# Performance work log

Measured on AMD Instinct MI355X. Metric: run time of the kernel, lower is better.

The kernel has to match this reference:

```python
import jax, jax.numpy as jnp
import numpy as np

B, D, H = 16384, 64, 128
L = D - 1  # number of per-dimension sub-networks (layers 1..dim-1)
W_SCALE = 0.05  # keep alpha outputs small so exp(alpha) stays well-conditioned


def setup_inputs() -> dict:
    key = jax.random.key(0)
    ks = jax.random.split(key, 8)
    return {
        "x": jax.random.normal(ks[0], (B, D), dtype=jnp.float32),
        "W1": jax.random.normal(ks[1], (L, D - 1, H), dtype=jnp.float32) * W_SCALE,
        "b1": jax.random.normal(ks[2], (L, H), dtype=jnp.float32) * W_SCALE,
        "W2": jax.random.normal(ks[3], (L, H, H), dtype=jnp.float32) * W_SCALE,
        "b2": jax.random.normal(ks[4], (L, H), dtype=jnp.float32) * W_SCALE,
        "W3": jax.random.normal(ks[5], (L, H, 2), dtype=jnp.float32) * W_SCALE,
        "b3": jax.random.normal(ks[6], (L, 2), dtype=jnp.float32) * W_SCALE,
        "initial_param": jax.random.uniform(
            ks[7], (2,), dtype=jnp.float32,
            minval=-np.sqrt(0.5), maxval=np.sqrt(0.5)),
    }


def reference(x, W1, b1, W2, b2, W3, b3, initial_param):
    # x: [B, D]. Layer l (l=0..L-1) corresponds to dim i=l+1 and consumes
    # x[:, :l+1]; we realize the ragged inputs via a triangular mask on W1.
    b, d = x.shape
    # mask[l, j] = 1 if input feature j is visible to layer l (j <= l)
    mask = (jnp.arange(d - 1)[None, :] <= jnp.arange(L)[:, None]).astype(x.dtype)
    W1m = W1 * mask[:, :, None]                       # [L, D-1, H]
    h = jnp.tanh(jnp.einsum('bd,ldh->blh', x[:, :d - 1], W1m) + b1)  # [B, L, H]
    h = jnp.tanh(jnp.einsum('blh,lhk->blk', h, W2) + b2)             # [B, L, H]
    out = jnp.einsum('blh,lho->blo', h, W3) + b3                     # [B, L, 2]
    mu0 = jnp.broadcast_to(initial_param[0], (b, 1))
    a0 = jnp.broadcast_to(initial_param[1], (b, 1))
    mu = jnp.concatenate([mu0, out[..., 0]], axis=1)   # [B, D]
    alpha = jnp.concatenate([a0, out[..., 1]], axis=1)  # [B, D]
    z = (x - mu) * jnp.exp(-alpha)
    log_det = -jnp.sum(alpha, axis=1)                  # [B]
    return z[:, ::-1], log_det
```

## Files before the change

### kernel.cpp

```cpp
#include <hip/hip_runtime.h>
#include <hip/hip_bf16.h>
#include <stdint.h>

#define B_N   16384
#define D_N   64
#define L_N   63
#define H_N   128
#define K2LOG2E 2.8853900817779268f

typedef unsigned int   u32;
typedef unsigned short u16;
typedef __attribute__((ext_vector_type(8))) __bf16 bf16x8;
typedef __attribute__((ext_vector_type(4))) float  f32x4;

__device__ __forceinline__ u16 f2b(float f){
  u32 u = __builtin_bit_cast(u32, f);
  u += 0x7fffu + ((u >> 16) & 1u);
  return (u16)(u >> 16);
}
__device__ __forceinline__ u32 pk_bf16(float lo, float hi){
  u32 r;
  asm("v_cvt_pk_bf16_f32 %0, %1, %2" : "=v"(r) : "v"(lo), "v"(hi));
  return r;
}
__device__ __forceinline__ float tanh_b(float acc, float bb){
  float t = __builtin_amdgcn_exp2f(fmaf(acc, K2LOG2E, bb));
  float r = __builtin_amdgcn_rcpf(t + 1.0f);
  return fmaf(-2.0f, r, 1.0f);
}

__global__ void k_conv_w1(const float* __restrict__ W1, u16* __restrict__ out){
  __shared__ u16 t[128*64];
  const int l = blockIdx.x, tid = threadIdx.x;
  #pragma unroll
  for (int i = 0; i < 32; ++i) t[i*256 + tid] = 0;
  __syncthreads();
  for (int i = 0; i < 32; ++i){
    int idx = i*256 + tid;
    if (idx < 63*128){
      int d = idx >> 7, n = idx & 127;
      if (d <= l) t[n*64 + d] = f2b(W1[(l*63 + d)*128 + n]);
    }
  }
  __syncthreads();
  uint4* o = (uint4*)(out + l*(128*64));
  const uint4* s4 = (const uint4*)t;
  #pragma unroll
  for (int i = 0; i < 4; ++i) o[i*256 + tid] = s4[i*256 + tid];
}

__global__ void k_conv_w2(const float* __restrict__ W2, u16* __restrict__ out){
  __shared__ u16 t[128*128];
  const int l = blockIdx.x, tid = threadIdx.x;
  #pragma unroll
  for (int i = 0; i < 64; ++i){
    int idx = i*256 + tid;
    int h = idx >> 7, k = idx & 127;
    t[k*128 + h] = f2b(W2[l*16384 + idx]);
  }
  __syncthreads();
  uint4* o = (uint4*)(out + l*(128*128));
  const uint4* s4 = (const uint4*)t;
  #pragma unroll
  for (int i = 0; i < 8; ++i) o[i*256 + tid] = s4[i*256 + tid];
}

__global__ void k_conv_x(const float* __restrict__ x, u16* __restrict__ out){
  int idx = blockIdx.x*256 + threadIdx.x;
  float4 v = ((const float4*)x)[idx];
  ushort4 r;
  r.x = f2b(v.x); r.y = f2b(v.y); r.z = f2b(v.z); r.w = f2b(v.w);
  ((ushort4*)out)[idx] = r;
}

__global__ __launch_bounds__(256, 2)
void k_main(const u16* __restrict__ W1T, const u16* __restrict__ W2T,
            const u16* __restrict__ xbf, const float* __restrict__ b1,
            const float* __restrict__ b2, const float* __restrict__ W3,
            const float* __restrict__ b3, float* __restrict__ mu,
            float* __restrict__ alpha)
{
  __shared__ __align__(16) char lds[26624];
  const int tid = threadIdx.x;
  const int l  = blockIdx.y;
  const int bx = blockIdx.x;
  const int wv = tid >> 6;
  const int ln = tid & 63;
  const int c  = ln & 15;
  const int g  = ln >> 4;

  {
    const uint4* xg = (const uint4*)(xbf + (size_t)bx * 64 * 64);
    #pragma unroll
    for (int i = 0; i < 2; ++i){
      int q = tid*2 + i;
      int row = q >> 3, cq = q & 7;
      uint4 v = xg[q];
      *(uint4*)(lds + row*128 + ((cq*16) ^ ((row&7)<<4))) = v;
    }
  }

  const u16* w1p = W1T + l * (128*64);
  const u16* w2p = W2T + l * (128*128);

  bf16x8 a1[2][2];
  #pragma unroll
  for (int m = 0; m < 2; ++m)
    #pragma unroll
    for (int s = 0; s < 2; ++s)
      a1[m][s] = *(const bf16x8*)(w1p + ((2*wv+m)*16 + c)*64 + s*32 + g*8);

  float bb1[2][4], bb2[2][4], w30[2][4], w31[2][4];
  #pragma unroll
  for (int m = 0; m < 2; ++m){
    int h0 = (2*wv+m)*16 + g*4;
    #pragma unroll
    for (int r = 0; r < 4; ++r){
      bb1[m][r] = b1[l*128 + h0 + r] * K2LOG2E;
      bb2[m][r] = b2[l*128 + h0 + r] * K2LOG2E;
      float2 w3v = ((const float2*)W3)[l*128 + h0 + r];
      w30[m][r] = w3v.x; w31[m][r] = w3v.y;
    }
  }

  __syncthreads();

  f32x4 acc1[2][4] = {};
  #pragma unroll
  for (int s = 0; s < 2; ++s){
    bf16x8 bfr[4];
    #pragma unroll
    for (int bt = 0; bt < 4; ++bt){
      int b = bt*16 + c;
      bfr[bt] = *(const bf16x8*)(lds + b*128 + ((s*64 + g*16) ^ ((b&7)<<4)));
    }
    #pragma unroll
    for (int m = 0; m < 2; ++m)
      #pragma unroll
      for (int bt = 0; bt < 4; ++bt)
        acc1[m][bt] = __builtin_amdgcn_mfma_f32_16x16x32_bf16(a1[m][s], bfr[bt], acc1[m][bt], 0, 0, 0);
  }

  #pragma unroll
  for (int m = 0; m < 2; ++m){
    int h0 = (2*wv+m)*16 + g*4;
    #pragma unroll
    for (int bt = 0; bt < 4; ++bt){
      float y0 = tanh_b(acc1[m][bt][0], bb1[m][0]);
      float y1 = tanh_b(acc1[m][bt][1], bb1[m][1]);
      float y2 = tanh_b(acc1[m][bt][2], bb1[m][2]);
      float y3 = tanh_b(acc1[m][bt][3], bb1[m][3]);
      u32 p0 = pk_bf16(y0, y1);
      u32 p1 = pk_bf16(y2, y3);
      int b = bt*16 + c;
      *(uint2*)(lds + 8192 + b*256 + ((h0*2) ^ ((b&7)<<4))) = make_uint2(p0, p1);
    }
  }
  __syncthreads();

  f32x4 acc2[2][4] = {};
  #pragma unroll
  for (int s = 0; s < 4; ++s){
    bf16x8 bfr[4];
    #pragma unroll
    for (int bt = 0; bt < 4; ++bt){
      int b = bt*16 + c;
      bfr[bt] = *(const bf16x8*)(lds + 8192 + b*256 + ((s*64 + g*16) ^ ((b&7)<<4)));
    }
    #pragma unroll
    for (int m = 0; m < 2; ++m){
      bf16x8 a = *(const bf16x8*)(w2p + ((2*wv+m)*16 + c)*128 + s*32 + g*8);
      #pragma unroll
      for (int bt = 0; bt < 4; ++bt)
        acc2[m][bt] = __builtin_amdgcn_mfma_f32_16x16x32_bf16(a, bfr[bt], acc2[m][bt], 0, 0, 0);
    }
  }

  float part[4][2] = {{0.f,0.f},{0.f,0.f},{0.f,0.f},{0.f,0.f}};
  #pragma unroll
  for (int m = 0; m < 2; ++m){
    #pragma unroll
    for (int bt = 0; bt < 4; ++bt)
      #pragma unroll
      for (int r = 0; r < 4; ++r){
        float h2 = tanh_b(acc2[m][bt][r], bb2[m][r]);
        part[bt][0] = fmaf(h2, w30[m][r], part[bt][0]);
        part[bt][1] = fmaf(h2, w31[m][r], part[bt][1]);
      }
  }
  #pragma unroll
  for (int bt = 0; bt < 4; ++bt)
    #pragma unroll
    for (int o = 0; o < 2; ++o){
      float v = part[bt][o];
      v += __shfl_xor(v, 16, 64);
      v += __shfl_xor(v, 32, 64);
      part[bt][o] = v;
    }
  float* sc = (float*)(lds + 24576);
  if (g == 0){
    #pragma unroll
    for (int bt = 0; bt < 4; ++bt){
      sc[(wv*64 + bt*16 + c)*2 + 0] = part[bt][0];
      sc[(wv*64 + bt*16 + c)*2 + 1] = part[bt][1];
    }
  }
  __syncthreads();
  if (tid < 128){
    int b = tid >> 1, o = tid & 1;
    float sum = sc[b*2+o] + sc[(64+b)*2+o] + sc[(128+b)*2+o] + sc[(192+b)*2+o]
              + b3[l*2 + o];
    int row = bx*64 + b;
    if (o == 0) mu[row*64 + l + 1]    = sum;
    else        alpha[row*64 + l + 1] = sum;
  }
}

__global__ void k_fin(const float* __restrict__ x, const float* __restrict__ mu,
                      const float* __restrict__ alpha, const float* __restrict__ ip,
                      float* __restrict__ out)
{
  int row = blockIdx.x*4 + (threadIdx.x >> 6);
  int d   = threadIdx.x & 63;
  float xv = x[row*64 + d];
  float m  = (d == 0) ? ip[0] : mu[row*64 + d];
  float a  = (d == 0) ? ip[1] : alpha[row*64 + d];
  float z  = (xv - m) * __expf(-a);
  out[row*64 + 63 - d] = z;
  float s = a;
  #pragma unroll
  for (int off = 32; off; off >>= 1) s += __shfl_xor(s, off, 64);
  if (d == 0) out[B_N*D_N + row] = -s;
}

extern "C" void kernel_launch(void* const* d_in, const int* in_sizes, int n_in,
                              void* d_out, int out_size, void* d_ws, size_t ws_size,
                              hipStream_t stream)
{
  const float* x  = (const float*)d_in[0];
  const float* W1 = (const float*)d_in[1];
  const float* b1 = (const float*)d_in[2];
  const float* W2 = (const float*)d_in[3];
  const float* b2 = (const float*)d_in[4];
  const float* W3 = (const float*)d_in[5];
  const float* b3 = (const float*)d_in[6];
  const float* ip = (const float*)d_in[7];

  char* ws = (char*)d_ws;
  u16*   w1t  = (u16*)(ws);
  u16*   w2t  = (u16*)(ws + 1048576);
  u16*   xbf  = (u16*)(ws + 1048576 + 2097152);
  float* mu   = (float*)(ws + 5242880);
  float* alph = (float*)(ws + 9437184);
  if (ws_size < 13631488) return;

  k_conv_w1<<<L_N, 256, 0, stream>>>(W1, w1t);
  k_conv_w2<<<L_N, 256, 0, stream>>>(W2, w2t);
  k_conv_x<<<(B_N*D_N/4)/256, 256, 0, stream>>>(x, xbf);

  dim3 grid(B_N/64, L_N);
  k_main<<<grid, 256, 0, stream>>>(w1t, w2t, xbf, b1, b2, W3, b3, mu, alph);

  k_fin<<<B_N/4, 256, 0, stream>>>(x, mu, alph, ip, (float*)d_out);
}
```

Before: 148.8 us.

## Fold biases into GEMMs, do W3 via MFMA, fuse finalize with atomics

Biases b1 and b2 are folded into the bf16 weight matrices. For b1 a constant-one column replaces x[:,63], which the masked layers never use. For b2 an extra K chunk is multiplied by a one-hot vector. The W3 projection now runs as an MFMA instead of scalar FMAs, shuffles and a cross-wave LDS reduction. Each wave works on its own 16 rows with per-wave LDS and no block barriers, and occupancy is raised to 4 blocks per CU. The finalize kernel and the mu/alpha intermediate buffers are gone: z is written directly and log_det is accumulated with atomicAdd, which adds atomic contention across 63 layers and bf16 rounding of the biases and of W3.

```diff
diff --git a/kernel.cpp b/kernel.cpp
--- a/kernel.cpp
+++ b/kernel.cpp
@@ -3,10 +3,9 @@
 #include <stdint.h>
 
 #define B_N   16384
-#define D_N   64
 #define L_N   63
-#define H_N   128
 #define K2LOG2E 2.8853900817779268f
+#define LOG2E   1.4426950408889634f
 
 typedef unsigned int   u32;
 typedef unsigned short u16;
@@ -23,13 +22,14 @@
   asm("v_cvt_pk_bf16_f32 %0, %1, %2" : "=v"(r) : "v"(lo), "v"(hi));
   return r;
 }
-__device__ __forceinline__ float tanh_b(float acc, float bb){
-  float t = __builtin_amdgcn_exp2f(fmaf(acc, K2LOG2E, bb));
+__device__ __forceinline__ float tanh_pre(float a){
+  float t = __builtin_amdgcn_exp2f(a * K2LOG2E);
   float r = __builtin_amdgcn_rcpf(t + 1.0f);
   return fmaf(-2.0f, r, 1.0f);
 }
 
-__global__ void k_conv_w1(const float* __restrict__ W1, u16* __restrict__ out){
+__global__ void k_conv_w1(const float* __restrict__ W1, const float* __restrict__ b1,
+                          u16* __restrict__ out){
   __shared__ u16 t[128*64];
   const int l = blockIdx.x, tid = threadIdx.x;
   #pragma unroll
@@ -42,6 +42,7 @@
       if (d <= l) t[n*64 + d] = f2b(W1[(l*63 + d)*128 + n]);
     }
   }
+  if (tid < 128) t[tid*64 + 63] = f2b(b1[l*128 + tid]);
   __syncthreads();
   uint4* o = (uint4*)(out + l*(128*64));
   const uint4* s4 = (const uint4*)t;
@@ -49,188 +50,147 @@
   for (int i = 0; i < 4; ++i) o[i*256 + tid] = s4[i*256 + tid];
 }
 
-__global__ void k_conv_w2(const float* __restrict__ W2, u16* __restrict__ out){
-  __shared__ u16 t[128*128];
+__global__ void k_conv_w2(const float* __restrict__ W2, const float* __restrict__ b2,
+                          u16* __restrict__ out){
+  __shared__ u16 t[128*160];
   const int l = blockIdx.x, tid = threadIdx.x;
+  #pragma unroll
+  for (int i = 0; i < 80; ++i) t[i*256 + tid] = 0;
+  __syncthreads();
   #pragma unroll
   for (int i = 0; i < 64; ++i){
     int idx = i*256 + tid;
-    int h = idx >> 7, k = idx & 127;
-    t[k*128 + h] = f2b(W2[l*16384 + idx]);
-  }
-  __syncthreads();
-  uint4* o = (uint4*)(out + l*(128*128));
+    int h = idx >> 7, n = idx & 127;
+    t[n*160 + h] = f2b(W2[l*16384 + idx]);
+  }
+  if (tid < 128) t[tid*160 + 128] = f2b(b2[l*128 + tid]);
+  __syncthreads();
+  uint4* o = (uint4*)(out + l*(128*160));
   const uint4* s4 = (const uint4*)t;
   #pragma unroll
-  for (int i = 0; i < 8; ++i) o[i*256 + tid] = s4[i*256 + tid];
+  for (int i = 0; i < 10; ++i) o[i*256 + tid] = s4[i*256 + tid];
+}
+
+__global__ void k_conv_w3(const float* __restrict__ W3, u16* __restrict__ out){
+  __shared__ u16 t[16*128];
+  const int l = blockIdx.x, tid = threadIdx.x;
+  #pragma unroll
+  for (int i = 0; i < 8; ++i) t[i*256 + tid] = 0;
+  __syncthreads();
+  if (tid < 128){
+    t[tid]       = f2b(W3[l*256 + tid*2 + 0]);
+    t[128 + tid] = f2b(W3[l*256 + tid*2 + 1]);
+  }
+  __syncthreads();
+  uint4* o = (uint4*)(out + l*(16*128));
+  o[tid] = ((const uint4*)t)[tid];
 }
 
 __global__ void k_conv_x(const float* __restrict__ x, u16* __restrict__ out){
   int idx = blockIdx.x*256 + threadIdx.x;
   float4 v = ((const float4*)x)[idx];
   ushort4 r;
-  r.x = f2b(v.x); r.y = f2b(v.y); r.z = f2b(v.z); r.w = f2b(v.w);
+  r.x = f2b(v.x); r.y = f2b(v.y); r.z = f2b(v.z);
+  r.w = ((idx & 15) == 15) ? (u16)0x3F80 : f2b(v.w);
   ((ushort4*)out)[idx] = r;
 }
 
-__global__ __launch_bounds__(256, 2)
+__global__ void k_init(const float* __restrict__ x, const float* __restrict__ ip,
+                       float* __restrict__ out){
+  int row = blockIdx.x*256 + threadIdx.x;
+  float z = (x[(size_t)row*64] - ip[0]) * __builtin_amdgcn_exp2f(-ip[1]*LOG2E);
+  out[(size_t)row*64 + 63] = z;
+  out[(size_t)B_N*64 + row] = -ip[1];
+}
+
+__global__ __launch_bounds__(256, 4)
 void k_main(const u16* __restrict__ W1T, const u16* __restrict__ W2T,
-            const u16* __restrict__ xbf, const float* __restrict__ b1,
-            const float* __restrict__ b2, const float* __restrict__ W3,
-            const float* __restrict__ b3, float* __restrict__ mu,
-            float* __restrict__ alpha)
+            const u16* __restrict__ W3T, const u16* __restrict__ xbf,
+            const float* __restrict__ x, const float* __restrict__ b3,
+            float* __restrict__ out)
 {
-  __shared__ __align__(16) char lds[26624];
+  __shared__ __align__(16) char lds[16384];
   const int tid = threadIdx.x;
   const int l  = blockIdx.y;
-  const int bx = blockIdx.x;
   const int wv = tid >> 6;
   const int ln = tid & 63;
   const int c  = ln & 15;
   const int g  = ln >> 4;
-
-  {
-    const uint4* xg = (const uint4*)(xbf + (size_t)bx * 64 * 64);
+  const int rowbase = blockIdx.x*64 + wv*16;
+
+  char* const my  = lds + wv*4096 + c*256;
+  const int swz = c & 7;
+
+  const u16* xrow = xbf + (size_t)(rowbase + c)*64;
+  bf16x8 xf0 = *(const bf16x8*)(xrow + g*8);
+  bf16x8 xf1 = *(const bf16x8*)(xrow + 32 + g*8);
+
+  const u16* w1p = W1T + l*(128*64);
+  f32x4 acc1[8] = {};
+  #pragma unroll
+  for (int mt = 0; mt < 8; ++mt){
+    const u16* ap = w1p + (mt*16 + c)*64 + g*8;
+    bf16x8 a0 = *(const bf16x8*)(ap);
+    bf16x8 a1 = *(const bf16x8*)(ap + 32);
+    acc1[mt] = __builtin_amdgcn_mfma_f32_16x16x32_bf16(a0, xf0, acc1[mt], 0,0,0);
+    acc1[mt] = __builtin_amdgcn_mfma_f32_16x16x32_bf16(a1, xf1, acc1[mt], 0,0,0);
+  }
+
+  #pragma unroll
+  for (int mt = 0; mt < 8; ++mt){
+    u32 p0 = pk_bf16(tanh_pre(acc1[mt][0]), tanh_pre(acc1[mt][1]));
+    u32 p1 = pk_bf16(tanh_pre(acc1[mt][2]), tanh_pre(acc1[mt][3]));
+    int chunk = (mt*2 + (g>>1)) ^ swz;
+    *(uint2*)(my + chunk*16 + (g&1)*8) = make_uint2(p0, p1);
+  }
+
+  bf16x8 hf[4];
+  #pragma unroll
+  for (int s = 0; s < 4; ++s)
+    hf[s] = *(const bf16x8*)(my + (((s*4 + g) ^ swz) << 4));
+  uint4 cw; cw.x = (g == 0) ? 0x00003F80u : 0u; cw.y = cw.z = cw.w = 0u;
+  bf16x8 cf = __builtin_bit_cast(bf16x8, cw);
+
+  const u16* w2p = W2T + l*(128*160);
+  f32x4 acc2[8] = {};
+  #pragma unroll
+  for (int mt = 0; mt < 8; ++mt){
+    const u16* ap = w2p + (mt*16 + c)*160 + g*8;
     #pragma unroll
-    for (int i = 0; i < 2; ++i){
-      int q = tid*2 + i;
-      int row = q >> 3, cq = q & 7;
-      uint4 v = xg[q];
-      *(uint4*)(lds + row*128 + ((cq*16) ^ ((row&7)<<4))) = v;
+    for (int s = 0; s < 4; ++s){
+      bf16x8 a = *(const bf16x8*)(ap + s*32);
+      acc2[mt] = __builtin_amdgcn_mfma_f32_16x16x32_bf16(a, hf[s], acc2[mt], 0,0,0);
     }
-  }
-
-  const u16* w1p = W1T + l * (128*64);
-  const u16* w2p = W2T + l * (128*128);
-
-  bf16x8 a1[2][2];
-  #pragma unroll
-  for (int m = 0; m < 2; ++m)
-    #pragma unroll
-    for (int s = 0; s < 2; ++s)
-      a1[m][s] = *(const bf16x8*)(w1p + ((2*wv+m)*16 + c)*64 + s*32 + g*8);
-
-  float bb1[2][4], bb2[2][4], w30[2][4], w31[2][4];
-  #pragma unroll
-  for (int m = 0; m < 2; ++m){
-    int h0 = (2*wv+m)*16 + g*4;
-    #pragma unroll
-    for (int r = 0; r < 4; ++r){
-      bb1[m][r] = b1[l*128 + h0 + r] * K2LOG2E;
-      bb2[m][r] = b2[l*128 + h0 + r] * K2LOG2E;
-      float2 w3v = ((const float2*)W3)[l*128 + h0 + r];
-      w30[m][r] = w3v.x; w31[m][r] = w3v.y;
-    }
-  }
-
-  __syncthreads();
-
-  f32x4 acc1[2][4] = {};
-  #pragma unroll
-  for (int s = 0; s < 2; ++s){
-    bf16x8 bfr[4];
-    #pragma unroll
-    for (int bt = 0; bt < 4; ++bt){
-      int b = bt*16 + c;
-      bfr[bt] = *(const bf16x8*)(lds + b*128 + ((s*64 + g*16) ^ ((b&7)<<4)));
-    }
-    #pragma unroll
-    for (int m = 0; m < 2; ++m)
-      #pragma unroll
-      for (int bt = 0; bt < 4; ++bt)
-        acc1[m][bt] = __builtin_amdgcn_mfma_f32_16x16x32_bf16(a1[m][s], bfr[bt], acc1[m][bt], 0, 0, 0);
-  }
-
-  #pragma unroll
-  for (int m = 0; m < 2; ++m){
-    int h0 = (2*wv+m)*16 + g*4;
-    #pragma unroll
-    for (int bt = 0; bt < 4; ++bt){
-      float y0 = tanh_b(acc1[m][bt][0], bb1[m][0]);
-      float y1 = tanh_b(acc1[m][bt][1], bb1[m][1]);
-      float y2 = tanh_b(acc1[m][bt][2], bb1[m][2]);
-      float y3 = tanh_b(acc1[m][bt][3], bb1[m][3]);
-      u32 p0 = pk_bf16(y0, y1);
-      u32 p1 = pk_bf16(y2, y3);
-      int b = bt*16 + c;
-      *(uint2*)(lds + 8192 + b*256 + ((h0*2) ^ ((b&7)<<4))) = make_uint2(p0, p1);
-    }
-  }
-  __syncthreads();
-
-  f32x4 acc2[2][4] = {};
+    bf16x8 ab = *(const bf16x8*)(ap + 128);
+    acc2[mt] = __builtin_amdgcn_mfma_f32_16x16x32_bf16(ab, cf, acc2[mt], 0,0,0);
+  }
+
+  #pragma unroll
+  for (int mt = 0; mt < 8; ++mt){
+    u32 p0 = pk_bf16(tanh_pre(acc2[mt][0]), tanh_pre(acc2[mt][1]));
+    u32 p1 = pk_bf16(tanh_pre(acc2[mt][2]), tanh_pre(acc2[mt][3]));
+    int chunk = (mt*2 + (g>>1)) ^ swz;
+    *(uint2*)(my + chunk*16 + (g&1)*8) = make_uint2(p0, p1);
+  }
+
+  const u16* w3p = W3T + l*(16*128);
+  f32x4 acc3 = {};
   #pragma unroll
   for (int s = 0; s < 4; ++s){
-    bf16x8 bfr[4];
-    #pragma unroll
-    for (int bt = 0; bt < 4; ++bt){
-      int b = bt*16 + c;
-      bfr[bt] = *(const bf16x8*)(lds + 8192 + b*256 + ((s*64 + g*16) ^ ((b&7)<<4)));
-    }
-    #pragma unroll
-    for (int m = 0; m < 2; ++m){
-      bf16x8 a = *(const bf16x8*)(w2p + ((2*wv+m)*16 + c)*128 + s*32 + g*8);
-      #pragma unroll
-      for (int bt = 0; bt < 4; ++bt)
-        acc2[m][bt] = __builtin_amdgcn_mfma_f32_16x16x32_bf16(a, bfr[bt], acc2[m][bt], 0, 0, 0);
-    }
-  }
-
-  float part[4][2] = {{0.f,0.f},{0.f,0.f},{0.f,0.f},{0.f,0.f}};
-  #pragma unroll
-  for (int m = 0; m < 2; ++m){
-    #pragma unroll
-    for (int bt = 0; bt < 4; ++bt)
-      #pragma unroll
-      for (int r = 0; r < 4; ++r){
-        float h2 = tanh_b(acc2[m][bt][r], bb2[m][r]);
-        part[bt][0] = fmaf(h2, w30[m][r], part[bt][0]);
-        part[bt][1] = fmaf(h2, w31[m][r], part[bt][1]);
-      }
-  }
-  #pragma unroll
-  for (int bt = 0; bt < 4; ++bt)
-    #pragma unroll
-    for (int o = 0; o < 2; ++o){
-      float v = part[bt][o];
-      v += __shfl_xor(v, 16, 64);
-      v += __shfl_xor(v, 32, 64);
-      part[bt][o] = v;
-    }
-  float* sc = (float*)(lds + 24576);
+    bf16x8 hb = *(const bf16x8*)(my + (((s*4 + g) ^ swz) << 4));
+    bf16x8 a  = *(const bf16x8*)(w3p + c*128 + s*32 + g*8);
+    acc3 = __builtin_amdgcn_mfma_f32_16x16x32_bf16(a, hb, acc3, 0,0,0);
+  }
+
   if (g == 0){
-    #pragma unroll
-    for (int bt = 0; bt < 4; ++bt){
-      sc[(wv*64 + bt*16 + c)*2 + 0] = part[bt][0];
-      sc[(wv*64 + bt*16 + c)*2 + 1] = part[bt][1];
-    }
-  }
-  __syncthreads();
-  if (tid < 128){
-    int b = tid >> 1, o = tid & 1;
-    float sum = sc[b*2+o] + sc[(64+b)*2+o] + sc[(128+b)*2+o] + sc[(192+b)*2+o]
-              + b3[l*2 + o];
-    int row = bx*64 + b;
-    if (o == 0) mu[row*64 + l + 1]    = sum;
-    else        alpha[row*64 + l + 1] = sum;
-  }
-}
-
-__global__ void k_fin(const float* __restrict__ x, const float* __restrict__ mu,
-                      const float* __restrict__ alpha, const float* __restrict__ ip,
-                      float* __restrict__ out)
-{
-  int row = blockIdx.x*4 + (threadIdx.x >> 6);
-  int d   = threadIdx.x & 63;
-  float xv = x[row*64 + d];
-  float m  = (d == 0) ? ip[0] : mu[row*64 + d];
-  float a  = (d == 0) ? ip[1] : alpha[row*64 + d];
-  float z  = (xv - m) * __expf(-a);
-  out[row*64 + 63 - d] = z;
-  float s = a;
-  #pragma unroll
-  for (int off = 32; off; off >>= 1) s += __shfl_xor(s, off, 64);
-  if (d == 0) out[B_N*D_N + row] = -s;
+    int row = rowbase + c;
+    float muv = acc3[0] + b3[l*2 + 0];
+    float alv = acc3[1] + b3[l*2 + 1];
+    float xv  = x[(size_t)row*64 + (l + 1)];
+    float z   = (xv - muv) * __builtin_amdgcn_exp2f(-alv * LOG2E);
+    out[(size_t)row*64 + (62 - l)] = z;
+    atomicAdd(out + (size_t)B_N*64 + row, -alv);
+  }
 }
 
 extern "C" void kernel_launch(void* const* d_in, const int* in_sizes, int n_in,
@@ -247,19 +207,18 @@
   const float* ip = (const float*)d_in[7];
 
   char* ws = (char*)d_ws;
-  u16*   w1t  = (u16*)(ws);
-  u16*   w2t  = (u16*)(ws + 1048576);
-  u16*   xbf  = (u16*)(ws + 1048576 + 2097152);
-  float* mu   = (float*)(ws + 5242880);
-  float* alph = (float*)(ws + 9437184);
-  if (ws_size < 13631488) return;
-
-  k_conv_w1<<<L_N, 256, 0, stream>>>(W1, w1t);
-  k_conv_w2<<<L_N, 256, 0, stream>>>(W2, w2t);
-  k_conv_x<<<(B_N*D_N/4)/256, 256, 0, stream>>>(x, xbf);
+  u16* w1t = (u16*)(ws);
+  u16* w2t = (u16*)(ws + 1048576);
+  u16* w3t = (u16*)(ws + 3670016);
+  u16* xbf = (u16*)(ws + 3932160);
+  if (ws_size < 6029312) return;
+
+  k_conv_w1<<<L_N, 256, 0, stream>>>(W1, b1, w1t);
+  k_conv_w2<<<L_N, 256, 0, stream>>>(W2, b2, w2t);
+  k_conv_w3<<<L_N, 256, 0, stream>>>(W3, w3t);
+  k_conv_x<<<(B_N*64/4)/256, 256, 0, stream>>>(x, xbf);
+  k_init<<<B_N/256, 256, 0, stream>>>(x, ip, (float*)d_out);
 
   dim3 grid(B_N/64, L_N);
-  k_main<<<grid, 256, 0, stream>>>(w1t, w2t, xbf, b1, b2, W3, b3, mu, alph);
-
-  k_fin<<<B_N/4, 256, 0, stream>>>(x, mu, alph, ip, (float*)d_out);
-}
+  k_main<<<grid, 256, 0, stream>>>(w1t, w2t, w3t, xbf, x, b3, (float*)d_out);
+}
```

Measured after the change: 327.3 us. 120% more time.

## Enlarge row tile, fold b1 into GEMM, and reduce outputs with atomics

Applied to the files above, without the earlier changes.

Each block now processes 128 rows instead of 64. The x tile is read from global memory straight into MFMA fragments instead of being staged in LDS. The b1 bias is folded into the first GEMM by placing a bf16 ones column at x's last position and b1 in W1's padded column 63. The cross-wave reduction through LDS is replaced with global atomicAdds into zeroed mu/alpha buffers, with b3 added in the final kernel. The two weight-conversion kernels are merged, and launch bounds go up to 4 blocks per CU, adding a memset and atomic traffic and rounding b1 to bf16.

```diff
diff --git a/kernel.cpp b/kernel.cpp
--- a/kernel.cpp
+++ b/kernel.cpp
@@ -3,10 +3,9 @@
 #include <stdint.h>
 
 #define B_N   16384
-#define D_N   64
 #define L_N   63
-#define H_N   128
 #define K2LOG2E 2.8853900817779268f
+#define LOG2E   1.4426950408889634f
 
 typedef unsigned int   u32;
 typedef unsigned short u16;
@@ -23,14 +22,21 @@
   asm("v_cvt_pk_bf16_f32 %0, %1, %2" : "=v"(r) : "v"(lo), "v"(hi));
   return r;
 }
+__device__ __forceinline__ float tanh_pre(float a){
+  float t = __builtin_amdgcn_exp2f(a * K2LOG2E);
+  float r = __builtin_amdgcn_rcpf(t + 1.0f);
+  return fmaf(-2.0f, r, 1.0f);
+}
 __device__ __forceinline__ float tanh_b(float acc, float bb){
   float t = __builtin_amdgcn_exp2f(fmaf(acc, K2LOG2E, bb));
   float r = __builtin_amdgcn_rcpf(t + 1.0f);
   return fmaf(-2.0f, r, 1.0f);
 }
 
-__global__ void k_conv_w1(const float* __restrict__ W1, u16* __restrict__ out){
-  __shared__ u16 t[128*64];
+__global__ void k_conv_w(const float* __restrict__ W1, const float* __restrict__ b1,
+                         const float* __restrict__ W2,
+                         u16* __restrict__ w1t, u16* __restrict__ w2t){
+  __shared__ u16 t[16384];
   const int l = blockIdx.x, tid = threadIdx.x;
   #pragma unroll
   for (int i = 0; i < 32; ++i) t[i*256 + tid] = 0;
@@ -42,45 +48,46 @@
       if (d <= l) t[n*64 + d] = f2b(W1[(l*63 + d)*128 + n]);
     }
   }
-  __syncthreads();
-  uint4* o = (uint4*)(out + l*(128*64));
-  const uint4* s4 = (const uint4*)t;
-  #pragma unroll
-  for (int i = 0; i < 4; ++i) o[i*256 + tid] = s4[i*256 + tid];
-}
-
-__global__ void k_conv_w2(const float* __restrict__ W2, u16* __restrict__ out){
-  __shared__ u16 t[128*128];
-  const int l = blockIdx.x, tid = threadIdx.x;
+  if (tid < 128) t[tid*64 + 63] = f2b(b1[l*128 + tid]);
+  __syncthreads();
+  {
+    uint4* o = (uint4*)(w1t + l*(128*64));
+    const uint4* s4 = (const uint4*)t;
+    #pragma unroll
+    for (int i = 0; i < 4; ++i) o[i*256 + tid] = s4[i*256 + tid];
+  }
+  __syncthreads();
   #pragma unroll
   for (int i = 0; i < 64; ++i){
     int idx = i*256 + tid;
-    int h = idx >> 7, k = idx & 127;
-    t[k*128 + h] = f2b(W2[l*16384 + idx]);
-  }
-  __syncthreads();
-  uint4* o = (uint4*)(out + l*(128*128));
-  const uint4* s4 = (const uint4*)t;
-  #pragma unroll
-  for (int i = 0; i < 8; ++i) o[i*256 + tid] = s4[i*256 + tid];
+    int h = idx >> 7, n = idx & 127;
+    t[n*128 + h] = f2b(W2[l*16384 + idx]);
+  }
+  __syncthreads();
+  {
+    uint4* o = (uint4*)(w2t + l*(128*128));
+    const uint4* s4 = (const uint4*)t;
+    #pragma unroll
+    for (int i = 0; i < 8; ++i) o[i*256 + tid] = s4[i*256 + tid];
+  }
 }
 
 __global__ void k_conv_x(const float* __restrict__ x, u16* __restrict__ out){
   int idx = blockIdx.x*256 + threadIdx.x;
   float4 v = ((const float4*)x)[idx];
   ushort4 r;
-  r.x = f2b(v.x); r.y = f2b(v.y); r.z = f2b(v.z); r.w = f2b(v.w);
+  r.x = f2b(v.x); r.y = f2b(v.y); r.z = f2b(v.z);
+  r.w = ((idx & 15) == 15) ? (u16)0x3F80 : f2b(v.w);
   ((ushort4*)out)[idx] = r;
 }
 
-__global__ __launch_bounds__(256, 2)
+__global__ __launch_bounds__(256, 4)
 void k_main(const u16* __restrict__ W1T, const u16* __restrict__ W2T,
-            const u16* __restrict__ xbf, const float* __restrict__ b1,
-            const float* __restrict__ b2, const float* __restrict__ W3,
-            const float* __restrict__ b3, float* __restrict__ mu,
-            float* __restrict__ alpha)
+            const u16* __restrict__ xbf, const float* __restrict__ b2,
+            const float* __restrict__ W3,
+            float* __restrict__ mu, float* __restrict__ alpha)
 {
-  __shared__ __align__(16) char lds[26624];
+  __shared__ __align__(16) u16 h1[128*128];
   const int tid = threadIdx.x;
   const int l  = blockIdx.y;
   const int bx = blockIdx.x;
@@ -88,108 +95,75 @@
   const int ln = tid & 63;
   const int c  = ln & 15;
   const int g  = ln >> 4;
-
-  {
-    const uint4* xg = (const uint4*)(xbf + (size_t)bx * 64 * 64);
-    #pragma unroll
-    for (int i = 0; i < 2; ++i){
-      int q = tid*2 + i;
-      int row = q >> 3, cq = q & 7;
-      uint4 v = xg[q];
-      *(uint4*)(lds + row*128 + ((cq*16) ^ ((row&7)<<4))) = v;
-    }
-  }
-
-  const u16* w1p = W1T + l * (128*64);
-  const u16* w2p = W2T + l * (128*128);
-
-  bf16x8 a1[2][2];
-  #pragma unroll
-  for (int m = 0; m < 2; ++m)
-    #pragma unroll
-    for (int s = 0; s < 2; ++s)
-      a1[m][s] = *(const bf16x8*)(w1p + ((2*wv+m)*16 + c)*64 + s*32 + g*8);
-
-  float bb1[2][4], bb2[2][4], w30[2][4], w31[2][4];
+  const int rowbase = bx*128;
+  const int sx = (c & 7) << 4;
+  char* const h1b = (char*)h1;
+
+  const u16* w1p = W1T + l*(128*64);
+  const u16* w2p = W2T + l*(128*128);
+
+  f32x4 acc[2][8] = {};
+  #pragma unroll
+  for (int s = 0; s < 2; ++s){
+    bf16x8 a0 = *(const bf16x8*)(w1p + ((2*wv+0)*16 + c)*64 + s*32 + g*8);
+    bf16x8 a1 = *(const bf16x8*)(w1p + ((2*wv+1)*16 + c)*64 + s*32 + g*8);
+    #pragma unroll
+    for (int bt = 0; bt < 8; ++bt){
+      bf16x8 xf = *(const bf16x8*)(xbf + (size_t)(rowbase + bt*16 + c)*64 + s*32 + g*8);
+      acc[0][bt] = __builtin_amdgcn_mfma_f32_16x16x32_bf16(a0, xf, acc[0][bt], 0,0,0);
+      acc[1][bt] = __builtin_amdgcn_mfma_f32_16x16x32_bf16(a1, xf, acc[1][bt], 0,0,0);
+    }
+  }
+
   #pragma unroll
   for (int m = 0; m < 2; ++m){
     int h0 = (2*wv+m)*16 + g*4;
     #pragma unroll
+    for (int bt = 0; bt < 8; ++bt){
+      u32 p0 = pk_bf16(tanh_pre(acc[m][bt][0]), tanh_pre(acc[m][bt][1]));
+      u32 p1 = pk_bf16(tanh_pre(acc[m][bt][2]), tanh_pre(acc[m][bt][3]));
+      int b = bt*16 + c;
+      *(uint2*)(h1b + b*256 + ((h0*2) ^ sx)) = make_uint2(p0, p1);
+    }
+  }
+  __syncthreads();
+
+  f32x4 acc2[2][8] = {};
+  #pragma unroll
+  for (int s = 0; s < 4; ++s){
+    bf16x8 a0 = *(const bf16x8*)(w2p + ((2*wv+0)*16 + c)*128 + s*32 + g*8);
+    bf16x8 a1 = *(const bf16x8*)(w2p + ((2*wv+1)*16 + c)*128 + s*32 + g*8);
+    #pragma unroll
+    for (int bt = 0; bt < 8; ++bt){
+      int b = bt*16 + c;
+      bf16x8 hf = *(const bf16x8*)(h1b + b*256 + ((s*64 + g*16) ^ sx));
+      acc2[0][bt] = __builtin_amdgcn_mfma_f32_16x16x32_bf16(a0, hf, acc2[0][bt], 0,0,0);
+      acc2[1][bt] = __builtin_amdgcn_mfma_f32_16x16x32_bf16(a1, hf, acc2[1][bt], 0,0,0);
+    }
+  }
+
+  float part[8][2] = {};
+  #pragma unroll
+  for (int m = 0; m < 2; ++m){
+    int n0 = (2*wv+m)*16 + g*4;
+    float bb[4], w30[4], w31[4];
+    #pragma unroll
     for (int r = 0; r < 4; ++r){
-      bb1[m][r] = b1[l*128 + h0 + r] * K2LOG2E;
-      bb2[m][r] = b2[l*128 + h0 + r] * K2LOG2E;
-      float2 w3v = ((const float2*)W3)[l*128 + h0 + r];
-      w30[m][r] = w3v.x; w31[m][r] = w3v.y;
-    }
-  }
-
-  __syncthreads();
-
-  f32x4 acc1[2][4] = {};
-  #pragma unroll
-  for (int s = 0; s < 2; ++s){
-    bf16x8 bfr[4];
-    #pragma unroll
-    for (int bt = 0; bt < 4; ++bt){
-      int b = bt*16 + c;
-      bfr[bt] = *(const bf16x8*)(lds + b*128 + ((s*64 + g*16) ^ ((b&7)<<4)));
-    }
-    #pragma unroll
-    for (int m = 0; m < 2; ++m)
-      #pragma unroll
-      for (int bt = 0; bt < 4; ++bt)
-        acc1[m][bt] = __builtin_amdgcn_mfma_f32_16x16x32_bf16(a1[m][s], bfr[bt], acc1[m][bt], 0, 0, 0);
-  }
-
-  #pragma unroll
-  for (int m = 0; m < 2; ++m){
-    int h0 = (2*wv+m)*16 + g*4;
-    #pragma unroll
-    for (int bt = 0; bt < 4; ++bt){
-      float y0 = tanh_b(acc1[m][bt][0], bb1[m][0]);
-      float y1 = tanh_b(acc1[m][bt][1], bb1[m][1]);
-      float y2 = tanh_b(acc1[m][bt][2], bb1[m][2]);
-      float y3 = tanh_b(acc1[m][bt][3], bb1[m][3]);
-      u32 p0 = pk_bf16(y0, y1);
-      u32 p1 = pk_bf16(y2, y3);
-      int b = bt*16 + c;
-      *(uint2*)(lds + 8192 + b*256 + ((h0*2) ^ ((b&7)<<4))) = make_uint2(p0, p1);
-    }
-  }
-  __syncthreads();
-
-  f32x4 acc2[2][4] = {};
-  #pragma unroll
-  for (int s = 0; s < 4; ++s){
-    bf16x8 bfr[4];
-    #pragma unroll
-    for (int bt = 0; bt < 4; ++bt){
-      int b = bt*16 + c;
-      bfr[bt] = *(const bf16x8*)(lds + 8192 + b*256 + ((s*64 + g*16) ^ ((b&7)<<4)));
-    }
-    #pragma unroll
-    for (int m = 0; m < 2; ++m){
-      bf16x8 a = *(const bf16x8*)(w2p + ((2*wv+m)*16 + c)*128 + s*32 + g*8);
-      #pragma unroll
-      for (int bt = 0; bt < 4; ++bt)
-        acc2[m][bt] = __builtin_amdgcn_mfma_f32_16x16x32_bf16(a, bfr[bt], acc2[m][bt], 0, 0, 0);
-    }
-  }
-
-  float part[4][2] = {{0.f,0.f},{0.f,0.f},{0.f,0.f},{0.f,0.f}};
-  #pragma unroll
-  for (int m = 0; m < 2; ++m){
-    #pragma unroll
-    for (int bt = 0; bt < 4; ++bt)
+      bb[r] = b2[l*128 + n0 + r] * K2LOG2E;
+      float2 w3v = ((const float2*)W3)[l*128 + n0 + r];
+      w30[r] = w3v.x; w31[r] = w3v.y;
+    }
+    #pragma unroll
+    for (int bt = 0; bt < 8; ++bt)
       #pragma unroll
       for (int r = 0; r < 4; ++r){
-        float h2 = tanh_b(acc2[m][bt][r], bb2[m][r]);
-        part[bt][0] = fmaf(h2, w30[m][r], part[bt][0]);
-        part[bt][1] = fmaf(h2, w31[m][r], part[bt][1]);
+        float h2 = tanh_b(acc2[m][bt][r], bb[r]);
+        part[bt][0] = fmaf(h2, w30[r], part[bt][0]);
+        part[bt][1] = fmaf(h2, w31[r], part[bt][1]);
       }
   }
   #pragma unroll
-  for (int bt = 0; bt < 4; ++bt)
+  for (int bt = 0; bt < 8; ++bt){
     #pragma unroll
     for (int o = 0; o < 2; ++o){
       float v = part[bt][o];
@@ -197,40 +171,36 @@
       v += __shfl_xor(v, 32, 64);
       part[bt][o] = v;
     }
-  float* sc = (float*)(lds + 24576);
+  }
   if (g == 0){
     #pragma unroll
-    for (int bt = 0; bt < 4; ++bt){
-      sc[(wv*64 + bt*16 + c)*2 + 0] = part[bt][0];
-      sc[(wv*64 + bt*16 + c)*2 + 1] = part[bt][1];
-    }
-  }
-  __syncthreads();
-  if (tid < 128){
-    int b = tid >> 1, o = tid & 1;
-    float sum = sc[b*2+o] + sc[(64+b)*2+o] + sc[(128+b)*2+o] + sc[(192+b)*2+o]
-              + b3[l*2 + o];
-    int row = bx*64 + b;
-    if (o == 0) mu[row*64 + l + 1]    = sum;
-    else        alpha[row*64 + l + 1] = sum;
+    for (int bt = 0; bt < 8; ++bt){
+      int row = rowbase + bt*16 + c;
+      atomicAdd(mu    + (size_t)row*64 + l + 1, part[bt][0]);
+      atomicAdd(alpha + (size_t)row*64 + l + 1, part[bt][1]);
+    }
   }
 }
 
 __global__ void k_fin(const float* __restrict__ x, const float* __restrict__ mu,
-                      const float* __restrict__ alpha, const float* __restrict__ ip,
-                      float* __restrict__ out)
+                      const float* __restrict__ alpha, const float* __restrict__ b3,
+                      const float* __restrict__ ip, float* __restrict__ out)
 {
   int row = blockIdx.x*4 + (threadIdx.x >> 6);
   int d   = threadIdx.x & 63;
-  float xv = x[row*64 + d];
-  float m  = (d == 0) ? ip[0] : mu[row*64 + d];
-  float a  = (d == 0) ? ip[1] : alpha[row*64 + d];
-  float z  = (xv - m) * __expf(-a);
-  out[row*64 + 63 - d] = z;
+  float xv = x[(size_t)row*64 + d];
+  float m, a;
+  if (d == 0){ m = ip[0]; a = ip[1]; }
+  else {
+    m = mu[(size_t)row*64 + d]    + b3[(d-1)*2 + 0];
+    a = alpha[(size_t)row*64 + d] + b3[(d-1)*2 + 1];
+  }
+  float z = (xv - m) * __builtin_amdgcn_exp2f(-a * LOG2E);
+  out[(size_t)row*64 + 63 - d] = z;
   float s = a;
   #pragma unroll
   for (int off = 32; off; off >>= 1) s += __shfl_xor(s, off, 64);
-  if (d == 0) out[B_N*D_N + row] = -s;
+  if (d == 0) out[(size_t)B_N*64 + row] = -s;
 }
 
 extern "C" void kernel_launch(void* const* d_in, const int* in_sizes, int n_in,
@@ -249,17 +219,17 @@
   char* ws = (char*)d_ws;
   u16*   w1t  = (u16*)(ws);
   u16*   w2t  = (u16*)(ws + 1048576);
-  u16*   xbf  = (u16*)(ws + 1048576 + 2097152);
+  u16*   xbf  = (u16*)(ws + 3145728);
   float* mu   = (float*)(ws + 5242880);
   float* alph = (float*)(ws + 9437184);
   if (ws_size < 13631488) return;
 
-  k_conv_w1<<<L_N, 256, 0, stream>>>(W1, w1t);
-  k_conv_w2<<<L_N, 256, 0, stream>>>(W2, w2t);
-  k_conv_x<<<(B_N*D_N/4)/256, 256, 0, stream>>>(x, xbf);
-
-  dim3 grid(B_N/64, L_N);
-  k_main<<<grid, 256, 0, stream>>>(w1t, w2t, xbf, b1, b2, W3, b3, mu, alph);
-
-  k_fin<<<B_N/4, 256, 0, stream>>>(x, mu, alph, ip, (float*)d_out);
-}
+  k_conv_w<<<L_N, 256, 0, stream>>>(W1, b1, W2, w1t, w2t);
+  k_conv_x<<<(B_N*64/4)/256, 256, 0, stream>>>(x, xbf);
+  hipMemsetAsync(mu, 0, 8388608, stream);
+
+  dim3 grid(B_N/128, L_N);
+  k_main<<<grid, 256, 0, stream>>>(w1t, w2t, xbf, b2, W3, mu, alph);
+
+  k_fin<<<B_N/4, 256, 0, stream>>>(x, mu, alph, b3, ip, (float*)d_out);
+}
```

Result: slower. 450.8 us (+202.9%).
